# Kernel optimization log

Hardware: AMD Instinct MI355X
Metric: run time of the kernel (lower is better)

## Reference

```python
import jax, jax.numpy as jnp
import numpy as np

B, CIN, L = 4, 128, 2048
D_MODEL, D_STATE, EXPAND, HEADDIM, NGROUPS = 256, 16, 3, 3, 1
D_INNER = EXPAND * D_MODEL            # 768
NHEADS = D_INNER // HEADDIM           # 256
CONV_DIM = D_INNER + 2 * NGROUPS * D_STATE   # 800
D_IN_PROJ = 2 * D_INNER + 2 * NGROUPS * D_STATE + NHEADS  # 1824
K_PROJ, D_CONV = 4, 4
EPS = 1e-5


def setup_inputs() -> dict:
    key = jax.random.key(0)
    ks = jax.random.split(key, 9)
    x = jax.random.normal(ks[0], (B, CIN, L), jnp.float32)
    proj_w = jax.random.normal(ks[1], (D_MODEL, CIN, K_PROJ), jnp.float32) / np.float32(np.sqrt(CIN * K_PROJ))
    in_proj_w = jax.random.normal(ks[2], (D_IN_PROJ, D_MODEL), jnp.float32) / np.float32(np.sqrt(D_MODEL))
    conv_w = jax.random.normal(ks[3], (CONV_DIM, 1, D_CONV), jnp.float32) / np.float32(np.sqrt(D_CONV))
    conv_b = jax.random.normal(ks[4], (CONV_DIM,), jnp.float32) * 0.01
    # dt_bias = inverse-softplus of dt ~ LogUniform[1e-3, 1e-1] (mamba2 init)
    u = jax.random.uniform(ks[5], (NHEADS,), jnp.float32)
    dt = jnp.exp(u * np.float32(np.log(0.1) - np.log(1e-3)) + np.float32(np.log(1e-3)))
    dt_bias = dt + jnp.log(-jnp.expm1(-dt))
    A_log = jnp.log(1.0 + 15.0 * jax.random.uniform(ks[6], (NHEADS,), jnp.float32))  # A in [-16,-1]
    D_skip = jnp.ones((NHEADS,), jnp.float32)
    norm_w = jnp.ones((D_INNER,), jnp.float32)
    out_proj_w = jax.random.normal(ks[7], (D_MODEL, D_INNER), jnp.float32) / np.float32(np.sqrt(D_INNER))
    return {"x": x, "proj_w": proj_w, "in_proj_w": in_proj_w, "conv_w": conv_w,
            "conv_b": conv_b, "dt_bias": dt_bias, "A_log": A_log, "D_skip": D_skip,
            "norm_w": norm_w, "out_proj_w": out_proj_w}


def _forward(x, proj_w, in_proj_w, conv_w, conv_b, dt_bias, A_log, D_skip, norm_w, out_proj_w):
    # outer Conv1d, padding='same' (k=4 -> left 1, right 2), no bias: (B,CIN,L)->(B,D_MODEL,L)
    h = jax.lax.conv_general_dilated(x, proj_w, (1,), [(1, 2)],
                                     dimension_numbers=("NCH", "OIH", "NCH"))
    u = h.transpose(0, 2, 1)                          # (B, L, d_model)
    zxbcdt = jnp.einsum("bld,ed->ble", u, in_proj_w)  # (B, L, 1824)
    z = zxbcdt[..., :D_INNER]                                     # (B,L,768)
    xBC = zxbcdt[..., D_INNER:D_INNER + CONV_DIM]                 # (B,L,800)
    dt = zxbcdt[..., D_INNER + CONV_DIM:]                         # (B,L,256)
    dt = jax.nn.softplus(dt + dt_bias)
    # depthwise causal conv (pad d_conv-1 on left) + SiLU
    xBC_c = jax.lax.conv_general_dilated(xBC.transpose(0, 2, 1), conv_w, (1,), [(D_CONV - 1, 0)],
                                         feature_group_count=CONV_DIM,
                                         dimension_numbers=("NCH", "OIH", "NCH"))
    xBC = jax.nn.silu(xBC_c + conv_b[None, :, None]).transpose(0, 2, 1)  # (B,L,800)
    xs = xBC[..., :D_INNER].reshape(B, L, NHEADS, HEADDIM)        # (B,L,H,P)
    Bm = xBC[..., D_INNER:D_INNER + D_STATE]                      # (B,L,N) (ngroups=1)
    Cm = xBC[..., D_INNER + D_STATE:]                             # (B,L,N)
    A = -jnp.exp(A_log)                                           # (H,)

    def step(hst, inp):
        dt_t, x_t, B_t, C_t = inp                 # (B,H),(B,H,P),(B,N),(B,N)
        dA = jnp.exp(dt_t * A)[:, :, None, None]  # (B,H,1,1)
        hst = dA * hst + jnp.einsum("bh,bhp,bn->bhpn", dt_t, x_t, B_t)
        y_t = jnp.einsum("bhpn,bn->bhp", hst, C_t)
        return hst, y_t

    h0 = jnp.zeros((B, NHEADS, HEADDIM, D_STATE), x.dtype)
    _, ys = jax.lax.scan(step, h0, (dt.transpose(1, 0, 2), xs.transpose(1, 0, 2, 3),
                                    Bm.transpose(1, 0, 2), Cm.transpose(1, 0, 2)))
    y = ys.transpose(1, 0, 2, 3) + D_skip[None, None, :, None] * xs   # (B,L,H,P)
    y = y.reshape(B, L, D_INNER)
    # gated RMSNorm: gate first, then normalize (norm_before_gate=False)
    y = y * jax.nn.silu(z)
    y = y * jax.lax.rsqrt(jnp.mean(y * y, axis=-1, keepdims=True) + EPS) * norm_w
    out = jnp.einsum("ble,de->bld", y, out_proj_w)   # (B,L,d_model)
    return out.transpose(0, 2, 1)                    # (B,d_model,L)


def reference(x, proj_w, in_proj_w, conv_w, conv_b, dt_bias, A_log, D_skip, norm_w, out_proj_w):
    return _forward(x, proj_w, in_proj_w, conv_w, conv_b, dt_bias, A_log, D_skip, norm_w, out_proj_w)
```

## Files before the change

kernel.cpp:

```cpp
#include <hip/hip_runtime.h>
#include <hip/hip_fp16.h>
#include <math.h>

#define B_     4
#define CIN    128
#define LEN    2048
#define DMODEL 256
#define DSTATE 16
#define NHEADS 256
#define DINNER 768
#define CONVDIM 800
#define DINPROJ 1824
#define EPS_   1e-5f
#define CHUNK  64
#define NCHUNK 32

typedef _Float16 f16x8 __attribute__((ext_vector_type(8)));
typedef float    f32x4 __attribute__((ext_vector_type(4)));

__device__ __forceinline__ float silu_(float x){ return x / (1.0f + __expf(-x)); }
__device__ __forceinline__ float softplus_(float x){
    return x > 0.f ? x + log1pf(__expf(-x)) : log1pf(__expf(x));
}

__device__ __forceinline__ void gl2lds16(const _Float16* g, _Float16* l){
    __builtin_amdgcn_global_load_lds(
        (const __attribute__((address_space(1))) void*)g,
        (__attribute__((address_space(3))) void*)l, 16, 0, 0);
}

__global__ __launch_bounds__(256) void k_f2h3(const float* __restrict__ a0,
                                              const float* __restrict__ a1,
                                              const float* __restrict__ a2,
                                              _Float16* __restrict__ o0,
                                              _Float16* __restrict__ o1,
                                              _Float16* __restrict__ o2,
                                              int n0, int n1, int n2){
    int total = n0 + n1 + n2;
    for (int i = blockIdx.x * 256 + threadIdx.x; i < total; i += gridDim.x * 256){
        if (i < n0)            o0[i] = (_Float16)a0[i];
        else if (i < n0 + n1)  o1[i - n0] = (_Float16)a1[i - n0];
        else                   o2[i - n0 - n1] = (_Float16)a2[i - n0 - n1];
    }
}

__global__ __launch_bounds__(256) void k_im2col(const float* __restrict__ x,
                                                _Float16* __restrict__ xcol){
    __shared__ float xs[CIN][68];
    int blk = blockIdx.x;
    int b  = blk >> 5;
    int l0 = (blk & 31) << 6;
    const float* xb = x + (size_t)b * CIN * LEN;
    for (int idx = threadIdx.x; idx < CIN * 67; idx += 256){
        int ci = idx / 67, j = idx % 67;
        int gl = l0 - 1 + j;
        xs[ci][j] = (gl >= 0 && gl < LEN) ? xb[ci * LEN + gl] : 0.f;
    }
    __syncthreads();
    #pragma unroll
    for (int v = 0; v < 16; v++){
        int id = v * 256 + threadIdx.x;
        int rl = id >> 6, c = id & 63;
        f16x8 pk;
        #pragma unroll
        for (int e = 0; e < 8; e++){
            int ci = c * 2 + (e >> 2), k = e & 3;
            pk[e] = (_Float16)xs[ci][rl + k];
        }
        *(f16x8*)&xcol[((size_t)(b * LEN + l0 + rl)) * 512 + c * 8] = pk;
    }
}

template<int K, int EPI>
__global__ __launch_bounds__(256) void k_gemm(const _Float16* __restrict__ A,
                                              const _Float16* __restrict__ Bw,
                                              const float* __restrict__ dt_bias,
                                              _Float16* __restrict__ o_u,
                                              _Float16* __restrict__ o_z,
                                              _Float16* __restrict__ o_xbc,
                                              _Float16* __restrict__ o_dt,
                                              float* __restrict__ o_f){
    __shared__ __align__(16) _Float16 As[128 * 32];
    __shared__ __align__(16) _Float16 Bs[128 * 32];
    int tid  = threadIdx.x;
    int wv   = tid >> 6;
    int lane = tid & 63;
    int quad = lane >> 4;
    int l16  = lane & 15;
    int m0 = blockIdx.x * 128;
    int n0 = blockIdx.y * 128;
    int wm = (wv >> 1) * 64;
    int wn = (wv & 1) * 64;
    int srow = lane >> 2;
    int scol = (lane & 3) * 8;

    f32x4 acc[4][4];
    #pragma unroll
    for (int i = 0; i < 4; i++)
        #pragma unroll
        for (int j = 0; j < 4; j++)
            acc[i][j] = (f32x4){0.f, 0.f, 0.f, 0.f};

    for (int k0 = 0; k0 < K; k0 += 32){
        #pragma unroll
        for (int j = 0; j < 2; j++){
            int ar = m0 + wv * 32 + j * 16 + srow;
            gl2lds16(A + (size_t)ar * K + k0 + scol,
                     &As[(wv * 32 + j * 16) * 32]);
            int nr = n0 + wv * 32 + j * 16 + srow;
            if (EPI == 1) nr = nr > (DINPROJ - 1) ? (DINPROJ - 1) : nr;
            gl2lds16(Bw + (size_t)nr * K + k0 + scol,
                     &Bs[(wv * 32 + j * 16) * 32]);
        }
        __syncthreads();
        f16x8 af[4], bf[4];
        #pragma unroll
        for (int i = 0; i < 4; i++)
            af[i] = *(const f16x8*)&As[(wm + i * 16 + l16) * 32 + quad * 8];
        #pragma unroll
        for (int j = 0; j < 4; j++)
            bf[j] = *(const f16x8*)&Bs[(wn + j * 16 + l16) * 32 + quad * 8];
        #pragma unroll
        for (int i = 0; i < 4; i++)
            #pragma unroll
            for (int j = 0; j < 4; j++)
                acc[i][j] = __builtin_amdgcn_mfma_f32_16x16x32_f16(
                                af[i], bf[j], acc[i][j], 0, 0, 0);
        __syncthreads();
    }

    if (EPI == 0){
        #pragma unroll
        for (int j = 0; j < 4; j++){
            int col = n0 + wn + j * 16 + l16;
            #pragma unroll
            for (int i = 0; i < 4; i++){
                int row = m0 + wm + i * 16 + quad * 4;
                #pragma unroll
                for (int r = 0; r < 4; r++)
                    o_u[(size_t)(row + r) * DMODEL + col] = (_Float16)acc[i][j][r];
            }
        }
    } else if (EPI == 1){
        #pragma unroll
        for (int j = 0; j < 4; j++){
            int col = n0 + wn + j * 16 + l16;
            if (col < DINNER){
                #pragma unroll
                for (int i = 0; i < 4; i++){
                    int row = m0 + wm + i * 16 + quad * 4;
                    #pragma unroll
                    for (int r = 0; r < 4; r++)
                        o_z[(size_t)(row + r) * DINNER + col] = (_Float16)acc[i][j][r];
                }
            } else if (col < DINNER + CONVDIM){
                int cc = col - DINNER;
                #pragma unroll
                for (int i = 0; i < 4; i++){
                    int row = m0 + wm + i * 16 + quad * 4;
                    #pragma unroll
                    for (int r = 0; r < 4; r++)
                        o_xbc[(size_t)(row + r) * CONVDIM + cc] = (_Float16)acc[i][j][r];
                }
            } else if (col < DINPROJ){
                int hh = col - (DINNER + CONVDIM);
                float bias = dt_bias[hh];
                #pragma unroll
                for (int i = 0; i < 4; i++){
                    int row = m0 + wm + i * 16 + quad * 4;
                    #pragma unroll
                    for (int r = 0; r < 4; r++)
                        o_dt[(size_t)(row + r) * NHEADS + hh] =
                            (_Float16)softplus_(acc[i][j][r] + bias);
                }
            }
        }
    } else {
        #pragma unroll
        for (int i = 0; i < 4; i++){
            int row = m0 + wm + i * 16 + quad * 4;
            int b = row >> 11, l = row & (LEN - 1);
            #pragma unroll
            for (int j = 0; j < 4; j++){
                int d = n0 + wn + j * 16 + l16;
                *(f32x4*)&o_f[(((size_t)(b * DMODEL + d)) << 11) + l] = acc[i][j];
            }
        }
    }
}

__global__ __launch_bounds__(256) void k_dwconv(const __half* __restrict__ xbc,
                                                const float* __restrict__ cw,
                                                const float* __restrict__ cb,
                                                __half* __restrict__ xcc){
    int idx = blockIdx.x * 256 + threadIdx.x;
    int seg = idx % 100;
    int r   = idx / 100;
    int l   = r & (LEN - 1);
    int c8  = seg * 8;
    const _Float16* base = (const _Float16*)xbc + (size_t)r * CONVDIM + c8;
    f16x8 zv = {0, 0, 0, 0, 0, 0, 0, 0};
    f16x8 x3 = *(const f16x8*)base;
    f16x8 x2 = (l >= 1) ? *(const f16x8*)(base - CONVDIM) : zv;
    f16x8 x1 = (l >= 2) ? *(const f16x8*)(base - 2 * CONVDIM) : zv;
    f16x8 x0 = (l >= 3) ? *(const f16x8*)(base - 3 * CONVDIM) : zv;
    f16x8 o;
    #pragma unroll
    for (int e = 0; e < 8; e++){
        float4 wv = *(const float4*)(cw + (size_t)(c8 + e) * 4);
        float acc = cb[c8 + e]
                  + (float)x0[e] * wv.x + (float)x1[e] * wv.y
                  + (float)x2[e] * wv.z + (float)x3[e] * wv.w;
        o[e] = (_Float16)silu_(acc);
    }
    *(f16x8*)((_Float16*)xcc + (size_t)r * CONVDIM + c8) = o;
}

__global__ __launch_bounds__(256) void k_scanAC(const __half* __restrict__ dtb,
                                                const __half* __restrict__ xcc,
                                                const float* __restrict__ A_log,
                                                const float* __restrict__ D_skip,
                                                __half* __restrict__ y,
                                                __half* __restrict__ cstate,
                                                float* __restrict__ dsum){
    int wave = threadIdx.x >> 6;
    int task = blockIdx.x * 4 + wave;
    int c  = task & (NCHUNK - 1);
    int hg = (task >> 5) & 63;
    int b  = task >> 11;
    int lane = threadIdx.x & 63;
    int hl = lane >> 4;
    int n  = lane & 15;
    int h  = hg * 4 + hl;
    int c0 = h * 3;
    float A   = -__expf(A_log[h]);
    float Dsk = D_skip[h];
    int t0 = c * CHUNK;
    const __half* xr  = xcc + ((size_t)b * LEN + t0) * CONVDIM;
    const __half* dtp = dtb + ((size_t)b * LEN + t0) * NHEADS + h;
    float h0 = 0.f, h1 = 0.f, h2 = 0.f, sdt = 0.f;
    __half* yp = y + ((size_t)b * LEN + t0) * DINNER + c0;
    for (int t = 0; t < CHUNK; t++){
        float vx0 = __half2float(xr[c0]);
        float vx1 = __half2float(xr[c0 + 1]);
        float vx2 = __half2float(xr[c0 + 2]);
        float vB  = __half2float(xr[DINNER + n]);
        float vC  = __half2float(xr[DINNER + DSTATE + n]);
        float cdt = __half2float(dtp[(size_t)t * NHEADS]);
        float dA  = __expf(cdt * A);
        float dtB = cdt * vB;
        h0 = fmaf(h0, dA, vx0 * dtB);
        h1 = fmaf(h1, dA, vx1 * dtB);
        h2 = fmaf(h2, dA, vx2 * dtB);
        sdt += cdt;
        float p0 = h0 * vC, p1 = h1 * vC, p2 = h2 * vC;
        #pragma unroll
        for (int m = 1; m < 16; m <<= 1){
            p0 += __shfl_xor(p0, m, 64);
            p1 += __shfl_xor(p1, m, 64);
            p2 += __shfl_xor(p2, m, 64);
        }
        if (n < 3){
            float pv = (n == 0) ? p0 : ((n == 1) ? p1 : p2);
            float xv = (n == 0) ? vx0 : ((n == 1) ? vx1 : vx2);
            yp[n] = __float2half(fmaf(Dsk, xv, pv));
        }
        xr += CONVDIM;
        yp += DINNER;
    }
    size_t sbase = (((size_t)(b * NHEADS + h)) * NCHUNK + c) * 48;
    cstate[sbase + n]      = __float2half(h0);
    cstate[sbase + 16 + n] = __float2half(h1);
    cstate[sbase + 32 + n] = __float2half(h2);
    if (n == 0) dsum[(size_t)(b * NHEADS + h) * NCHUNK + c] = __expf(A * sdt);
}

__global__ __launch_bounds__(64) void k_scanB(__half* __restrict__ cstate,
                                              const float* __restrict__ dsum){
    int bh = blockIdx.x;
    int lane = threadIdx.x;
    if (lane >= 48) return;
    __half* st = cstate + (size_t)bh * NCHUNK * 48 + lane;
    const float* dd = dsum + (size_t)bh * NCHUNK;
    float H = 0.f;
    for (int c = 0; c < NCHUNK; c++){
        float d = dd[c];
        float s = __half2float(st[(size_t)c * 48]);
        st[(size_t)c * 48] = __float2half(H);
        H = fmaf(H, d, s);
    }
}

__global__ __launch_bounds__(256) void k_fixup(const __half* __restrict__ dtb,
                                               const __half* __restrict__ xcc,
                                               const float* __restrict__ A_log,
                                               const __half* __restrict__ cstate,
                                               __half* __restrict__ y){
    __shared__ __align__(16) _Float16 decay[32][256];
    __shared__ __align__(16) _Float16 Cs[32][16];
    int blk = blockIdx.x;
    int th = blk & 1;
    int c  = (blk >> 1) & 31;
    int b  = blk >> 6;
    int tid = threadIdx.x;
    int base_t = th * 32;
    size_t row0 = (size_t)b * LEN + c * CHUNK;

    if (tid < 64){
        int i = tid >> 1, k = tid & 1;
        *(f16x8*)&Cs[i][k * 8] =
            *(const f16x8*)((const _Float16*)xcc +
                            (row0 + base_t + i) * CONVDIM + DINNER + DSTATE + k * 8);
    }
    {
        float A = -__expf(A_log[tid]);
        float cum = 0.f;
        const _Float16* dp = (const _Float16*)dtb + row0 * NHEADS + tid;
        for (int t = 0; t < CHUNK; t++){
            cum += (float)dp[(size_t)t * NHEADS];
            if (t >= base_t && t < base_t + 32)
                decay[t - base_t][tid] = (_Float16)__expf(A * cum);
        }
    }
    __syncthreads();

    const _Float16* hp = (const _Float16*)cstate +
                         (((size_t)(b * NHEADS + tid)) * NCHUNK + c) * 48;
    float Hi[3][16];
    #pragma unroll
    for (int p = 0; p < 3; p++){
        f16x8 a = *(const f16x8*)(hp + p * 16);
        f16x8 bq = *(const f16x8*)(hp + p * 16 + 8);
        #pragma unroll
        for (int e = 0; e < 8; e++){ Hi[p][e] = (float)a[e]; Hi[p][8 + e] = (float)bq[e]; }
    }
    __half* yb = y + (row0 + base_t) * DINNER + tid * 3;
    for (int i = 0; i < 32; i++){
        float s0 = 0.f, s1 = 0.f, s2 = 0.f;
        #pragma unroll
        for (int nn = 0; nn < 16; nn++){
            float cv = (float)Cs[i][nn];
            s0 = fmaf(cv, Hi[0][nn], s0);
            s1 = fmaf(cv, Hi[1][nn], s1);
            s2 = fmaf(cv, Hi[2][nn], s2);
        }
        float d = (float)decay[i][tid];
        __half* yp = yb + (size_t)i * DINNER;
        yp[0] = __float2half(__half2float(yp[0]) + d * s0);
        yp[1] = __float2half(__half2float(yp[1]) + d * s1);
        yp[2] = __float2half(__half2float(yp[2]) + d * s2);
    }
}

__global__ __launch_bounds__(256) void k_norm(__half* __restrict__ y,
                                              const __half* __restrict__ z,
                                              const float* __restrict__ nw){
    __shared__ float wsum[4];
    size_t r = blockIdx.x;
    int tid = threadIdx.x;
    const __half* zr = z + r * DINNER;
    __half* yr = y + r * DINNER;
    int e0 = tid, e1 = tid + 256, e2 = tid + 512;
    float t0 = __half2float(yr[e0]) * silu_(__half2float(zr[e0]));
    float t1 = __half2float(yr[e1]) * silu_(__half2float(zr[e1]));
    float t2 = __half2float(yr[e2]) * silu_(__half2float(zr[e2]));
    float ss = t0 * t0 + t1 * t1 + t2 * t2;
    #pragma unroll
    for (int m = 1; m < 64; m <<= 1) ss += __shfl_xor(ss, m, 64);
    if ((tid & 63) == 0) wsum[tid >> 6] = ss;
    __syncthreads();
    float tot = wsum[0] + wsum[1] + wsum[2] + wsum[3];
    float sc = rsqrtf(tot / (float)DINNER + EPS_);
    yr[e0] = __float2half(t0 * sc * nw[e0]);
    yr[e1] = __float2half(t1 * sc * nw[e1]);
    yr[e2] = __float2half(t2 * sc * nw[e2]);
}

extern "C" void kernel_launch(void* const* d_in, const int* in_sizes, int n_in,
                              void* d_out, int out_size, void* d_ws, size_t ws_size,
                              hipStream_t stream) {
    const float* x          = (const float*)d_in[0];
    const float* proj_w     = (const float*)d_in[1];
    const float* in_proj_w  = (const float*)d_in[2];
    const float* conv_w     = (const float*)d_in[3];
    const float* conv_b     = (const float*)d_in[4];
    const float* dt_bias    = (const float*)d_in[5];
    const float* A_log      = (const float*)d_in[6];
    const float* D_skip     = (const float*)d_in[7];
    const float* norm_w     = (const float*)d_in[8];
    const float* out_proj_w = (const float*)d_in[9];
    float* out = (float*)d_out;

    char* ob = (char*)d_out;
    _Float16* pw_h  = (_Float16*)ob;
    _Float16* ipw_h = (_Float16*)(ob + 262144);

    char* wsb = (char*)d_ws;
    _Float16* xcol  = (_Float16*)(wsb);
    _Float16* u_h   = (_Float16*)(wsb + 8388608);
    __half*   xcc_h = (__half*)(wsb);
    __half*   z_h   = (__half*)(wsb + 13107200);
    __half*   xbc_h = (__half*)(wsb + 25690112);
    __half*   y_h   = xbc_h;
    __half*   dt_h  = (__half*)(wsb + 38797312);
    __half*   cstate= (__half*)(wsb + 42991616);
    float*    dsum  = (float*)(wsb + 46137344);
    _Float16* opw_h = (_Float16*)(wsb + 46268416);

    k_f2h3  <<<96, 256, 0, stream>>>(proj_w, in_proj_w, out_proj_w,
                                     pw_h, ipw_h, opw_h,
                                     DMODEL * CIN * 4, DINPROJ * DMODEL,
                                     DMODEL * DINNER);
    k_im2col<<<128, 256, 0, stream>>>(x, xcol);
    k_gemm<512, 0><<<dim3(64, 2), 256, 0, stream>>>(xcol, pw_h, nullptr,
        u_h, nullptr, nullptr, nullptr, nullptr);
    k_gemm<256, 1><<<dim3(64, 15), 256, 0, stream>>>(u_h, ipw_h, dt_bias,
        nullptr, (_Float16*)z_h, (_Float16*)xbc_h, (_Float16*)dt_h, nullptr);
    k_dwconv<<<3200, 256, 0, stream>>>(xbc_h, conv_w, conv_b, xcc_h);
    k_scanAC<<<2048, 256, 0, stream>>>(dt_h, xcc_h, A_log, D_skip, y_h, cstate, dsum);
    k_scanB <<<1024, 64, 0, stream>>>(cstate, dsum);
    k_fixup <<<256, 256, 0, stream>>>(dt_h, xcc_h, A_log, cstate, y_h);
    k_norm  <<<8192, 256, 0, stream>>>(y_h, z_h, norm_w);
    k_gemm<768, 2><<<dim3(64, 2), 256, 0, stream>>>((const _Float16*)y_h, opw_h,
        nullptr, nullptr, nullptr, nullptr, nullptr, out);
}
```

Before: 320.3 us.

## Replace sequential intra-chunk scan with quadratic SSD-style chunk computation; merge prep kernels

The per-timestep recurrent scan inside each chunk is replaced by an SSD-style quadratic form. Each block stages a 64-step chunk for 16 heads in LDS, builds the C·Bᵀ Gram matrix once and shares it across heads, and computes outputs as masked decay-weighted sums. Chunk-end states come from a weighted reduction over B and x. This removes the serial 64-step dependency chain and the per-step shuffle reductions, at the cost of more exp and FMA work and fp16 rounding of the Gram matrix. Separately, weight conversion and im2col are merged into one launch to save a kernel launch.

```diff
diff --git a/kernel.cpp b/kernel.cpp
--- a/kernel.cpp
+++ b/kernel.cpp
@@ -29,45 +29,46 @@
         (__attribute__((address_space(3))) void*)l, 16, 0, 0);
 }
 
-__global__ __launch_bounds__(256) void k_f2h3(const float* __restrict__ a0,
+__global__ __launch_bounds__(256) void k_prep(const float* __restrict__ x,
+                                              const float* __restrict__ a0,
                                               const float* __restrict__ a1,
                                               const float* __restrict__ a2,
                                               _Float16* __restrict__ o0,
                                               _Float16* __restrict__ o1,
                                               _Float16* __restrict__ o2,
-                                              int n0, int n1, int n2){
-    int total = n0 + n1 + n2;
-    for (int i = blockIdx.x * 256 + threadIdx.x; i < total; i += gridDim.x * 256){
-        if (i < n0)            o0[i] = (_Float16)a0[i];
-        else if (i < n0 + n1)  o1[i - n0] = (_Float16)a1[i - n0];
-        else                   o2[i - n0 - n1] = (_Float16)a2[i - n0 - n1];
-    }
-}
-
-__global__ __launch_bounds__(256) void k_im2col(const float* __restrict__ x,
-                                                _Float16* __restrict__ xcol){
+                                              _Float16* __restrict__ xcol){
     __shared__ float xs[CIN][68];
-    int blk = blockIdx.x;
-    int b  = blk >> 5;
-    int l0 = (blk & 31) << 6;
-    const float* xb = x + (size_t)b * CIN * LEN;
-    for (int idx = threadIdx.x; idx < CIN * 67; idx += 256){
-        int ci = idx / 67, j = idx % 67;
-        int gl = l0 - 1 + j;
-        xs[ci][j] = (gl >= 0 && gl < LEN) ? xb[ci * LEN + gl] : 0.f;
-    }
-    __syncthreads();
-    #pragma unroll
-    for (int v = 0; v < 16; v++){
-        int id = v * 256 + threadIdx.x;
-        int rl = id >> 6, c = id & 63;
-        f16x8 pk;
-        #pragma unroll
-        for (int e = 0; e < 8; e++){
-            int ci = c * 2 + (e >> 2), k = e & 3;
-            pk[e] = (_Float16)xs[ci][rl + k];
-        }
-        *(f16x8*)&xcol[((size_t)(b * LEN + l0 + rl)) * 512 + c * 8] = pk;
+    if (blockIdx.x < 128){
+        int blk = blockIdx.x;
+        int b  = blk >> 5;
+        int l0 = (blk & 31) << 6;
+        const float* xb = x + (size_t)b * CIN * LEN;
+        for (int idx = threadIdx.x; idx < CIN * 67; idx += 256){
+            int ci = idx / 67, j = idx % 67;
+            int gl = l0 - 1 + j;
+            xs[ci][j] = (gl >= 0 && gl < LEN) ? xb[ci * LEN + gl] : 0.f;
+        }
+        __syncthreads();
+        #pragma unroll
+        for (int v = 0; v < 16; v++){
+            int id = v * 256 + threadIdx.x;
+            int rl = id >> 6, c = id & 63;
+            f16x8 pk;
+            #pragma unroll
+            for (int e = 0; e < 8; e++){
+                int ci = c * 2 + (e >> 2), k = e & 3;
+                pk[e] = (_Float16)xs[ci][rl + k];
+            }
+            *(f16x8*)&xcol[((size_t)(b * LEN + l0 + rl)) * 512 + c * 8] = pk;
+        }
+    } else {
+        const int n0 = DMODEL * CIN * 4, n1 = DINPROJ * DMODEL, n2 = DMODEL * DINNER;
+        int total = n0 + n1 + n2;
+        for (int i = (blockIdx.x - 128) * 256 + threadIdx.x; i < total; i += 96 * 256){
+            if (i < n0)            o0[i] = (_Float16)a0[i];
+            else if (i < n0 + n1)  o1[i - n0] = (_Float16)a1[i - n0];
+            else                   o2[i - n0 - n1] = (_Float16)a2[i - n0 - n1];
+        }
     }
 }
 
@@ -216,63 +217,111 @@
     *(f16x8*)((_Float16*)xcc + (size_t)r * CONVDIM + c8) = o;
 }
 
-__global__ __launch_bounds__(256) void k_scanAC(const __half* __restrict__ dtb,
-                                                const __half* __restrict__ xcc,
-                                                const float* __restrict__ A_log,
-                                                const float* __restrict__ D_skip,
-                                                __half* __restrict__ y,
-                                                __half* __restrict__ cstate,
-                                                float* __restrict__ dsum){
-    int wave = threadIdx.x >> 6;
-    int task = blockIdx.x * 4 + wave;
-    int c  = task & (NCHUNK - 1);
-    int hg = (task >> 5) & 63;
-    int b  = task >> 11;
-    int lane = threadIdx.x & 63;
-    int hl = lane >> 4;
-    int n  = lane & 15;
-    int h  = hg * 4 + hl;
-    int c0 = h * 3;
-    float A   = -__expf(A_log[h]);
-    float Dsk = D_skip[h];
-    int t0 = c * CHUNK;
-    const __half* xr  = xcc + ((size_t)b * LEN + t0) * CONVDIM;
-    const __half* dtp = dtb + ((size_t)b * LEN + t0) * NHEADS + h;
-    float h0 = 0.f, h1 = 0.f, h2 = 0.f, sdt = 0.f;
-    __half* yp = y + ((size_t)b * LEN + t0) * DINNER + c0;
-    for (int t = 0; t < CHUNK; t++){
-        float vx0 = __half2float(xr[c0]);
-        float vx1 = __half2float(xr[c0 + 1]);
-        float vx2 = __half2float(xr[c0 + 2]);
-        float vB  = __half2float(xr[DINNER + n]);
-        float vC  = __half2float(xr[DINNER + DSTATE + n]);
-        float cdt = __half2float(dtp[(size_t)t * NHEADS]);
-        float dA  = __expf(cdt * A);
-        float dtB = cdt * vB;
-        h0 = fmaf(h0, dA, vx0 * dtB);
-        h1 = fmaf(h1, dA, vx1 * dtB);
-        h2 = fmaf(h2, dA, vx2 * dtB);
-        sdt += cdt;
-        float p0 = h0 * vC, p1 = h1 * vC, p2 = h2 * vC;
-        #pragma unroll
-        for (int m = 1; m < 16; m <<= 1){
-            p0 += __shfl_xor(p0, m, 64);
-            p1 += __shfl_xor(p1, m, 64);
-            p2 += __shfl_xor(p2, m, 64);
-        }
-        if (n < 3){
-            float pv = (n == 0) ? p0 : ((n == 1) ? p1 : p2);
-            float xv = (n == 0) ? vx0 : ((n == 1) ? vx1 : vx2);
-            yp[n] = __float2half(fmaf(Dsk, xv, pv));
-        }
-        xr += CONVDIM;
-        yp += DINNER;
-    }
-    size_t sbase = (((size_t)(b * NHEADS + h)) * NCHUNK + c) * 48;
-    cstate[sbase + n]      = __float2half(h0);
-    cstate[sbase + 16 + n] = __float2half(h1);
-    cstate[sbase + 32 + n] = __float2half(h2);
-    if (n == 0) dsum[(size_t)(b * NHEADS + h) * NCHUNK + c] = __expf(A * sdt);
+__global__ __launch_bounds__(256) void k_scanQ(const __half* __restrict__ dtb,
+                                               const __half* __restrict__ xcc,
+                                               const float* __restrict__ A_log,
+                                               const float* __restrict__ D_skip,
+                                               __half* __restrict__ y,
+                                               __half* __restrict__ cstate,
+                                               float* __restrict__ dsum){
+    __shared__ __align__(16) _Float16 xs_x[64][48];
+    __shared__ __align__(16) _Float16 xs_bc[64][32];
+    __shared__ __align__(16) _Float16 xs_dt[64][16];
+    __shared__ __align__(16) _Float16 Gs[64][66];
+    __shared__ __align__(16) float    xf[4][64][4];
+    __shared__ __align__(16) float    sv[4][64][2];
+    int blk = blockIdx.x;
+    int hg = blk & 15;
+    int c  = (blk >> 4) & 31;
+    int b  = blk >> 9;
+    int tid = threadIdx.x;
+    size_t row0 = (size_t)b * LEN + c * CHUNK;
+
+    const _Float16* xc16 = (const _Float16*)xcc;
+    const _Float16* dt16 = (const _Float16*)dtb;
+    #pragma unroll
+    for (int k = 0; k < 3; k++){
+        int seg = tid + k * 256;
+        if (seg < 384){
+            int t = seg / 6, k16 = seg % 6;
+            *(f16x8*)&xs_x[t][k16 * 8] =
+                *(const f16x8*)(xc16 + (row0 + t) * CONVDIM + hg * 48 + k16 * 8);
+        } else if (seg < 640){
+            int i = seg - 384; int t = i >> 2, k4 = i & 3;
+            *(f16x8*)&xs_bc[t][k4 * 8] =
+                *(const f16x8*)(xc16 + (row0 + t) * CONVDIM + DINNER + k4 * 8);
+        } else {
+            int i = seg - 640; int t = i >> 1, k2 = i & 1;
+            *(f16x8*)&xs_dt[t][k2 * 8] =
+                *(const f16x8*)(dt16 + (row0 + t) * NHEADS + hg * 16 + k2 * 8);
+        }
+    }
+    __syncthreads();
+
+    int w = tid >> 6, lane = tid & 63;
+    {
+        float Crow[16];
+        #pragma unroll
+        for (int n2 = 0; n2 < 16; n2++) Crow[n2] = (float)xs_bc[lane][16 + n2];
+        for (int s = w * 16; s < w * 16 + 16; s++){
+            float g = 0.f;
+            #pragma unroll
+            for (int n2 = 0; n2 < 16; n2++)
+                g = fmaf(Crow[n2], (float)xs_bc[s][n2], g);
+            Gs[lane][s] = (_Float16)g;
+        }
+    }
+    __syncthreads();
+
+    for (int q = 0; q < 4; q++){
+        int j = w * 4 + q;
+        int h = hg * 16 + j;
+        float A   = -__expf(A_log[h]);
+        float Dsk = D_skip[h];
+        float dts = (float)xs_dt[lane][j];
+        float cum = dts;
+        #pragma unroll
+        for (int m = 1; m < 64; m <<= 1){
+            float u = __shfl_up(cum, m, 64);
+            if (lane >= m) cum += u;
+        }
+        float cumA  = A * cum;
+        float cumAL = __shfl(cumA, 63, 64);
+        float x0 = (float)xs_x[lane][j * 3 + 0];
+        float x1 = (float)xs_x[lane][j * 3 + 1];
+        float x2 = (float)xs_x[lane][j * 3 + 2];
+        xf[w][lane][0] = x0; xf[w][lane][1] = x1;
+        xf[w][lane][2] = x2; xf[w][lane][3] = dts;
+        sv[w][lane][0] = cumA;
+        sv[w][lane][1] = __expf(cumAL - cumA) * dts;
+        float y0 = 0.f, y1 = 0.f, y2 = 0.f;
+        for (int s = 0; s < 64; s++){
+            float g = (float)Gs[lane][s];
+            f32x4 xv = *(const f32x4*)&xf[w][s][0];
+            float P = g * __expf(cumA - sv[w][s][0]) * xv[3];
+            P = (s <= lane) ? P : 0.f;
+            y0 = fmaf(P, xv[0], y0);
+            y1 = fmaf(P, xv[1], y1);
+            y2 = fmaf(P, xv[2], y2);
+        }
+        __half* yp = y + (row0 + lane) * DINNER + h * 3;
+        yp[0] = __float2half(fmaf(Dsk, x0, y0));
+        yp[1] = __float2half(fmaf(Dsk, x1, y1));
+        yp[2] = __float2half(fmaf(Dsk, x2, y2));
+        if (lane < 48){
+            int p = lane >> 4, n = lane & 15;
+            float hacc = 0.f;
+            for (int s = 0; s < 64; s++){
+                float wg = sv[w][s][1];
+                float Bv = (float)xs_bc[s][n];
+                hacc = fmaf(wg * Bv, xf[w][s][p], hacc);
+            }
+            size_t sbase = (((size_t)(b * NHEADS + h)) * NCHUNK + c) * 48;
+            cstate[sbase + lane] = __float2half(hacc);
+        }
+        if (lane == 0)
+            dsum[(size_t)(b * NHEADS + h) * NCHUNK + c] = __expf(cumAL);
+    }
 }
 
 __global__ __launch_bounds__(64) void k_scanB(__half* __restrict__ cstate,
@@ -407,17 +456,14 @@
     float*    dsum  = (float*)(wsb + 46137344);
     _Float16* opw_h = (_Float16*)(wsb + 46268416);
 
-    k_f2h3  <<<96, 256, 0, stream>>>(proj_w, in_proj_w, out_proj_w,
-                                     pw_h, ipw_h, opw_h,
-                                     DMODEL * CIN * 4, DINPROJ * DMODEL,
-                                     DMODEL * DINNER);
-    k_im2col<<<128, 256, 0, stream>>>(x, xcol);
+    k_prep  <<<224, 256, 0, stream>>>(x, proj_w, in_proj_w, out_proj_w,
+                                      pw_h, ipw_h, opw_h, xcol);
     k_gemm<512, 0><<<dim3(64, 2), 256, 0, stream>>>(xcol, pw_h, nullptr,
         u_h, nullptr, nullptr, nullptr, nullptr);
     k_gemm<256, 1><<<dim3(64, 15), 256, 0, stream>>>(u_h, ipw_h, dt_bias,
         nullptr, (_Float16*)z_h, (_Float16*)xbc_h, (_Float16*)dt_h, nullptr);
     k_dwconv<<<3200, 256, 0, stream>>>(xbc_h, conv_w, conv_b, xcc_h);
-    k_scanAC<<<2048, 256, 0, stream>>>(dt_h, xcc_h, A_log, D_skip, y_h, cstate, dsum);
+    k_scanQ <<<2048, 256, 0, stream>>>(dt_h, xcc_h, A_log, D_skip, y_h, cstate, dsum);
     k_scanB <<<1024, 64, 0, stream>>>(cstate, dsum);
     k_fixup <<<256, 256, 0, stream>>>(dt_h, xcc_h, A_log, cstate, y_h);
     k_norm  <<<8192, 256, 0, stream>>>(y_h, z_h, norm_w);
```

Result: slower. 356.7 us (+11.4%).
